# Performance work log

Measured on AMD Instinct MI355X. Metric: run time of the kernel, lower is better.

## Reference

```python
import jax, jax.numpy as jnp
import numpy as np


def setup_inputs() -> dict:
    key = jax.random.key(0)
    ks = jax.random.split(key, 7)
    B, S, D, F, E = 4, 2048, 1024, 4096, 8
    scale = 0.02
    return {
        "x": jax.random.normal(ks[0], (B, S, D), dtype=jnp.float32),
        "gate_w": jax.random.normal(ks[1], (D, E), dtype=jnp.float32) * scale,
        "gate_b": jnp.zeros((E,), dtype=jnp.float32),
        "w1": jax.random.normal(ks[2], (E, D, F), dtype=jnp.float32) * scale,
        "b1": jnp.zeros((E, F), dtype=jnp.float32),
        "w2": jax.random.normal(ks[3], (E, F, D), dtype=jnp.float32) * scale,
        "b2": jnp.zeros((E, D), dtype=jnp.float32),
        "top_k": 2,
    }


def reference(x, gate_w, gate_b, w1, b1, w2, b2, top_k):
    B, S, D = x.shape
    E = w1.shape[0]
    xf = x.reshape(-1, D)                      # [T, D], T = B*S
    T = xf.shape[0]

    # Router: top-k logits, softmax over the selected k (as in torch code)
    logits = xf @ gate_w + gate_b              # [T, E]
    rw, sel = jax.lax.top_k(logits, top_k)     # [T, k], [T, k]
    w = jax.nn.softmax(rw, axis=-1)            # [T, k]

    # Dense combine weights: combine[t, e] = sum_k w[t,k] * (sel[t,k]==e)
    combine = jnp.zeros((T, E), dtype=xf.dtype)
    combine = combine.at[jnp.arange(T)[:, None], sel].add(w)

    # Loop over small fixed expert count; each expert FFN on all tokens,
    # weighted by combine (zero for unrouted tokens). Dropout p honored as 0 (eval).
    out = jnp.zeros_like(xf)
    for e in range(E):
        h = jax.nn.gelu(xf @ w1[e] + b1[e], approximate=False)  # torch F.gelu = exact
        out = out + combine[:, e:e + 1] * (h @ w2[e] + b2[e])
    return out.reshape(B, S, D)
```

## Files before the change

kernel.cpp:

```cpp
#include <hip/hip_runtime.h>
#include <math.h>

#define T_TOK 8192
#define DDIM  1024
#define FDIM  4096
#define NEXP  8
#define MT256 72
#define NSLOT (2 * T_TOK)

typedef __attribute__((ext_vector_type(8))) short short8;
typedef __attribute__((ext_vector_type(4))) float f32x4;
typedef unsigned short u16;
typedef unsigned int   u32;

typedef const __attribute__((address_space(1))) u32* gp_t;
typedef       __attribute__((address_space(3))) u32* lp_t;

__device__ __forceinline__ void gload16(const void* g, void* l) {
  __builtin_amdgcn_global_load_lds((gp_t)g, (lp_t)l, 16, 0, 0);
}

#define VM0 asm volatile("s_waitcnt vmcnt(0)" ::: "memory")
#define SBAR __builtin_amdgcn_s_barrier()
#define SCHED0 __builtin_amdgcn_sched_barrier(0)

__device__ __forceinline__ u16 f2bf(float f) {
  u32 u = __float_as_uint(f);
  u = u + 0x7FFFu + ((u >> 16) & 1u);
  return (u16)(u >> 16);
}

__device__ __forceinline__ int imin(int a, int b) { return a < b ? a : b; }

__device__ __forceinline__ float gelu_fast(float v) {
  float u = 0.7978845608f * (v + 0.044715f * v * v * v);
  float t2 = __expf(2.f * u);
  float th = 1.f - 2.f / (t2 + 1.f);
  return 0.5f * v * (1.f + th);
}

__device__ __forceinline__ int xcd_swz(int orig, int nwg) {
  int xcd = orig & 7;
  int q = nwg >> 3, r = nwg & 7;
  int base = (xcd < r) ? xcd * (q + 1) : r * (q + 1) + (xcd - r) * q;
  return base + (orig >> 3);
}

__global__ __launch_bounds__(256) void router_kernel(
    const float* __restrict__ x, const float* __restrict__ gw,
    const float* __restrict__ gb, u16* __restrict__ xb,
    int* __restrict__ counts, int* __restrict__ sel, float* __restrict__ wts)
{
  const int t    = blockIdx.x * 4 + (threadIdx.x >> 6);
  const int lane = threadIdx.x & 63;
  const float* xr = x + (size_t)t * DDIM;
  u16* xbr = xb + (size_t)t * DDIM;
  float lg[NEXP];
  #pragma unroll
  for (int e = 0; e < NEXP; e++) lg[e] = 0.f;
  #pragma unroll
  for (int i = 0; i < 4; i++) {
    int d0 = i * 256 + lane * 4;
    float4 v = *(const float4*)(xr + d0);
    ushort4 o;
    o.x = f2bf(v.x); o.y = f2bf(v.y); o.z = f2bf(v.z); o.w = f2bf(v.w);
    *(ushort4*)(xbr + d0) = o;
    const float* g = gw + (size_t)d0 * NEXP;
    #pragma unroll
    for (int e = 0; e < NEXP; e++)
      lg[e] += v.x * g[e] + v.y * g[NEXP + e] + v.z * g[2 * NEXP + e] + v.w * g[3 * NEXP + e];
  }
  #pragma unroll
  for (int off = 32; off > 0; off >>= 1) {
    #pragma unroll
    for (int e = 0; e < NEXP; e++) lg[e] += __shfl_down(lg[e], off);
  }
  if (lane == 0) {
    float v0 = -1e30f, v1 = -1e30f; int s0 = 0, s1 = 0;
    #pragma unroll
    for (int e = 0; e < NEXP; e++) {
      float v = lg[e] + gb[e];
      if (v > v0) { v1 = v0; s1 = s0; v0 = v; s0 = e; }
      else if (v > v1) { v1 = v; s1 = e; }
    }
    float a  = expf(v1 - v0);
    float w0 = 1.f / (1.f + a);
    sel[t * 2] = s0; sel[t * 2 + 1] = s1;
    wts[t * 2] = w0; wts[t * 2 + 1] = 1.f - w0;
    atomicAdd(&counts[s0], 1); atomicAdd(&counts[s1], 1);
  }
}

__global__ __launch_bounds__(256) void scan_assign_kernel(
    const int* __restrict__ counts, const int* __restrict__ sel,
    const float* __restrict__ wts,
    int* __restrict__ offsets, int* __restrict__ map_e, int* __restrict__ map_r,
    int* __restrict__ nT, int* __restrict__ stok, float* __restrict__ swgt)
{
  __shared__ int spos[NEXP];
  if (threadIdx.x == 0) {
    int run = 0, nt = 0;
    for (int e = 0; e < NEXP; e++) {
      offsets[e] = run; spos[e] = run;
      int c = counts[e];
      int ntile = (c + 255) >> 8;
      for (int i = 0; i < ntile; i++) { map_e[nt] = e; map_r[nt] = i * 256; nt++; }
      run += c;
    }
    nT[0] = nt;
  }
  __syncthreads();
  for (int t = threadIdx.x; t < T_TOK; t += 256) {
    #pragma unroll
    for (int k = 0; k < 2; k++) {
      int e = sel[t * 2 + k];
      int p = atomicAdd(&spos[e], 1);
      stok[p] = t; swgt[p] = wts[t * 2 + k];
    }
  }
}

__global__ __launch_bounds__(256) void xgather_kernel(
    const u16* __restrict__ xb, const int* __restrict__ stok,
    u16* __restrict__ Xg)
{
  const int s = blockIdx.x * 2 + (threadIdx.x >> 7);
  const int u = threadIdx.x & 127;
  int tok = stok[s]; if ((u32)tok >= T_TOK) tok = 0;
  const uint4* src = (const uint4*)(xb + (size_t)tok * DDIM);
  uint4* dst = (uint4*)(Xg + (size_t)s * DDIM);
  dst[u] = src[u];
}

__global__ __launch_bounds__(256) void wtrans_kernel(
    const float* __restrict__ in, u16* __restrict__ out, int M, int N)
{
  const int e = blockIdx.z;
  in  += (size_t)e * M * N;
  out += (size_t)e * M * N;
  const int r0 = blockIdx.y * 128;
  const int c0 = blockIdx.x * 64;
  __shared__ float tile[128][65];
  const int tid = threadIdx.x;
  const int lr = tid >> 4;
  const int lc = (tid & 15) * 4;
  #pragma unroll
  for (int p = 0; p < 8; p++) {
    int r = p * 16 + lr;
    float4 v = *(const float4*)(in + (size_t)(r0 + r) * N + (c0 + lc));
    tile[r][lc] = v.x; tile[r][lc + 1] = v.y; tile[r][lc + 2] = v.z; tile[r][lc + 3] = v.w;
  }
  __syncthreads();
  const int oc = tid >> 4;
  const int om = (tid & 15) * 8;
  #pragma unroll
  for (int p = 0; p < 4; p++) {
    int c = p * 16 + oc;
    short8 o;
    #pragma unroll
    for (int j = 0; j < 8; j++) o[j] = (short)f2bf(tile[om + j][c]);
    *(short8*)(out + (size_t)(c0 + c) * M + (r0 + om)) = o;
  }
}

__global__ __launch_bounds__(512, 2) void gemm1_kernel(
    const u16* __restrict__ Xg, const u16* __restrict__ W1T,
    const float* __restrict__ B1,
    const int* __restrict__ counts, const int* __restrict__ offsets,
    const int* __restrict__ map_e, const int* __restrict__ map_r,
    const int* __restrict__ nT, u16* __restrict__ H)
{
  __shared__ __align__(16) char lds[2 * 65536];
  const int gid   = xcd_swz(blockIdx.x, gridDim.x);
  const int n_idx = gid / MT256;
  const int t_idx = gid - n_idx * MT256;
  if (t_idx >= nT[0]) return;
  const int e    = map_e[t_idx];
  const int row0 = map_r[t_idx];
  const int cnt  = counts[e];
  const int off  = offsets[e];
  const int n0   = n_idx * 256;

  const int tid = threadIdx.x, wave = tid >> 6, lane = tid & 63;
  const int lr = lane & 15, lq = lane >> 4;
  const int wr = wave >> 2, wc = wave & 3;
  const int l3 = lane >> 3;
  const int usrc = (lane & 7) ^ l3;

  const char* gA[4]; const char* gB[4];
  #pragma unroll
  for (int i = 0; i < 4; i++) {
    int rA = imin(off + row0 + wave * 32 + i * 8 + l3, NSLOT - 1);
    gA[i] = (const char*)Xg + (size_t)rA * 2048 + usrc * 16;
    int rB = e * FDIM + n0 + wave * 32 + i * 8 + l3;
    gB[i] = (const char*)W1T + (size_t)rB * 2048 + usrc * 16;
  }
  const int dbase = wave * 4096 + lane * 16;

  auto stage = [&](int buf, int kByte) {
    #pragma unroll
    for (int i = 0; i < 4; i++)
      gload16(gA[i] + kByte, lds + buf * 65536 + dbase + i * 1024);
    #pragma unroll
    for (int i = 0; i < 4; i++)
      gload16(gB[i] + kByte, lds + buf * 65536 + 32768 + dbase + i * 1024);
  };

  f32x4 acc[8][4] = {};
  auto compute = [&](int buf) {
    const u16* A  = (const u16*)(lds + buf * 65536);
    const u16* Bp = (const u16*)(lds + buf * 65536 + 32768);
    #pragma unroll
    for (int ks = 0; ks < 2; ks++) {
      const int uu = (((ks * 4 + lq) ^ (lr & 7))) * 8;
      short8 a[8], b[4];
      #pragma unroll
      for (int n = 0; n < 4; n++)
        b[n] = *(const short8*)&Bp[(wc * 64 + n * 16 + lr) * 64 + uu];
      #pragma unroll
      for (int m = 0; m < 8; m++)
        a[m] = *(const short8*)&A[(wr * 128 + m * 16 + lr) * 64 + uu];
      #pragma unroll
      for (int m = 0; m < 8; m++)
        #pragma unroll
        for (int n = 0; n < 4; n++)
          acc[m][n] = __builtin_amdgcn_mfma_f32_16x16x32_bf16(a[m], b[n], acc[m][n], 0, 0, 0);
    }
  };

  stage(0, 0);
  VM0; SCHED0; SBAR; SCHED0;
  #pragma unroll 1
  for (int t = 0; t < 16; t++) {
    if (t < 15) stage((t + 1) & 1, (t + 1) * 128);
    compute(t & 1);
    SCHED0; VM0; SCHED0; SBAR; SCHED0;
  }

  #pragma unroll
  for (int m = 0; m < 8; m++) {
    int rloc = wr * 128 + m * 16 + lq * 4;
    #pragma unroll
    for (int j = 0; j < 4; j++) {
      int r = rloc + j;
      if (row0 + r < cnt) {
        u16* Hrow = H + (size_t)(off + row0 + r) * FDIM;
        #pragma unroll
        for (int n = 0; n < 4; n++) {
          int col = n0 + wc * 64 + n * 16 + lr;
          float v = acc[m][n][j] + B1[e * FDIM + col];
          Hrow[col] = f2bf(gelu_fast(v));
        }
      }
    }
  }
}

__global__ __launch_bounds__(512, 2) void gemm2_kernel(
    const u16* __restrict__ H, const u16* __restrict__ W2T,
    const float* __restrict__ B2,
    const int* __restrict__ counts, const int* __restrict__ offsets,
    const int* __restrict__ slot_token, const float* __restrict__ slot_weight,
    const int* __restrict__ map_e, const int* __restrict__ map_r,
    const int* __restrict__ nT, float* __restrict__ out)
{
  __shared__ __align__(16) char lds[2 * 65536];
  const int gid   = xcd_swz(blockIdx.x, gridDim.x);
  const int sp    = gid / (4 * MT256);
  const int rem   = gid - sp * 4 * MT256;
  const int n_idx = rem / MT256;
  const int t_idx = rem - n_idx * MT256;
  if (t_idx >= nT[0]) return;
  const int e    = map_e[t_idx];
  const int row0 = map_r[t_idx];
  const int cnt  = counts[e];
  const int off  = offsets[e];
  const int n0   = n_idx * 256;
  const int kbase = sp * 4096;

  const int tid = threadIdx.x, wave = tid >> 6, lane = tid & 63;
  const int lr = lane & 15, lq = lane >> 4;
  const int wr = wave >> 2, wc = wave & 3;
  const int l3 = lane >> 3;
  const int usrc = (lane & 7) ^ l3;

  const char* gA[4]; const char* gB[4];
  #pragma unroll
  for (int i = 0; i < 4; i++) {
    int rA = imin(off + row0 + wave * 32 + i * 8 + l3, NSLOT - 1);
    gA[i] = (const char*)H + (size_t)rA * 8192 + kbase + usrc * 16;
    int rB = e * DDIM + n0 + wave * 32 + i * 8 + l3;
    gB[i] = (const char*)W2T + (size_t)rB * 8192 + kbase + usrc * 16;
  }
  const int dbase = wave * 4096 + lane * 16;

  auto stage = [&](int buf, int kByte) {
    #pragma unroll
    for (int i = 0; i < 4; i++)
      gload16(gA[i] + kByte, lds + buf * 65536 + dbase + i * 1024);
    #pragma unroll
    for (int i = 0; i < 4; i++)
      gload16(gB[i] + kByte, lds + buf * 65536 + 32768 + dbase + i * 1024);
  };

  f32x4 acc[8][4] = {};
  auto compute = [&](int buf) {
    const u16* A  = (const u16*)(lds + buf * 65536);
    const u16* Bp = (const u16*)(lds + buf * 65536 + 32768);
    #pragma unroll
    for (int ks = 0; ks < 2; ks++) {
      const int uu = (((ks * 4 + lq) ^ (lr & 7))) * 8;
      short8 a[8], b[4];
      #pragma unroll
      for (int n = 0; n < 4; n++)
        b[n] = *(const short8*)&Bp[(wc * 64 + n * 16 + lr) * 64 + uu];
      #pragma unroll
      for (int m = 0; m < 8; m++)
        a[m] = *(const short8*)&A[(wr * 128 + m * 16 + lr) * 64 + uu];
      #pragma unroll
      for (int m = 0; m < 8; m++)
        #pragma unroll
        for (int n = 0; n < 4; n++)
          acc[m][n] = __builtin_amdgcn_mfma_f32_16x16x32_bf16(a[m], b[n], acc[m][n], 0, 0, 0);
    }
  };

  stage(0, 0);
  VM0; SCHED0; SBAR; SCHED0;
  #pragma unroll 1
  for (int t = 0; t < 32; t++) {
    if (t < 31) stage((t + 1) & 1, (t + 1) * 128);
    compute(t & 1);
    SCHED0; VM0; SCHED0; SBAR; SCHED0;
  }

  #pragma unroll
  for (int m = 0; m < 8; m++) {
    int rloc = wr * 128 + m * 16 + lq * 4;
    #pragma unroll
    for (int j = 0; j < 4; j++) {
      int r = rloc + j;
      if (row0 + r >= cnt) continue;
      int s = off + row0 + r;
      int tok = slot_token[s];
      float wgt = slot_weight[s];
      #pragma unroll
      for (int n = 0; n < 4; n++) {
        int col = n0 + wc * 64 + n * 16 + lr;
        float v = acc[m][n][j];
        if (sp == 0) v += B2[e * DDIM + col];
        atomicAdd(&out[(size_t)tok * DDIM + col], wgt * v);
      }
    }
  }
}

extern "C" void kernel_launch(void* const* d_in, const int* in_sizes, int n_in,
                              void* d_out, int out_size, void* d_ws, size_t ws_size,
                              hipStream_t stream)
{
  (void)in_sizes; (void)n_in; (void)ws_size;
  const float* x  = (const float*)d_in[0];
  const float* gw = (const float*)d_in[1];
  const float* gb = (const float*)d_in[2];
  const float* w1 = (const float*)d_in[3];
  const float* b1 = (const float*)d_in[4];
  const float* w2 = (const float*)d_in[5];
  const float* b2 = (const float*)d_in[6];

  char* ws = (char*)d_ws;
  int*   counts = (int*)(ws + 0);
  int*   offp   = (int*)(ws + 64);
  int*   nT     = (int*)(ws + 128);
  int*   map_e  = (int*)(ws + 256);
  int*   map_r  = (int*)(ws + 1024);

  size_t p = 2048;
  int*   sel   = (int*)(ws + p);   p += (size_t)T_TOK * 2 * 4;
  float* wts   = (float*)(ws + p); p += (size_t)T_TOK * 2 * 4;
  int*   stok  = (int*)(ws + p);   p += (size_t)NSLOT * 4;
  float* swgt  = (float*)(ws + p); p += (size_t)NSLOT * 4;
  p = (p + 1048575) & ~(size_t)1048575;
  u16*   xb    = (u16*)(ws + p);   p += (size_t)T_TOK * DDIM * 2;
  u16*   Xg    = (u16*)(ws + p);   p += (size_t)NSLOT * DDIM * 2;
  u16*   w1t   = (u16*)(ws + p);   p += (size_t)NEXP * DDIM * FDIM * 2;
  u16*   w2t   = (u16*)(ws + p);   p += (size_t)NEXP * DDIM * FDIM * 2;
  u16*   Hbuf  = (u16*)(ws + p);

  hipMemsetAsync(ws, 0, 256, stream);
  hipMemsetAsync(d_out, 0, (size_t)out_size * sizeof(float), stream);
  router_kernel<<<T_TOK / 4, 256, 0, stream>>>(x, gw, gb, xb, counts, sel, wts);
  scan_assign_kernel<<<1, 256, 0, stream>>>(counts, sel, wts, offp, map_e, map_r, nT, stok, swgt);
  xgather_kernel<<<NSLOT / 2, 256, 0, stream>>>(xb, stok, Xg);
  wtrans_kernel<<<dim3(DDIM / 64, FDIM / 128, NEXP), 256, 0, stream>>>(w2, w2t, FDIM, DDIM);
  wtrans_kernel<<<dim3(FDIM / 64, DDIM / 128, NEXP), 256, 0, stream>>>(w1, w1t, DDIM, FDIM);

  gemm1_kernel<<<(FDIM / 256) * MT256, 512, 0, stream>>>(
      Xg, w1t, b1, counts, offp, map_e, map_r, nT, Hbuf);
  gemm2_kernel<<<2 * (DDIM / 256) * MT256, 512, 0, stream>>>(
      Hbuf, w2t, b2, counts, offp, stok, swgt, map_e, map_r, nT, (float*)d_out);
}
```

Baseline: 858.5 us.

## Use 128-row M tiles with triple-buffered LDS pipeline in expert GEMMs

Halves the token-tile height of both grouped GEMMs from 256 to 128 rows, so scan_assign emits 128-row tiles and the grids grow to a 136-tile maximum. This cuts padding waste on partially filled expert tiles and raises the block count. The LDS ring goes from two 64 KB buffers to three 48 KB slots, and loads are issued two stages ahead with a partial vmcnt wait instead of draining fully each step. In exchange, each B tile is loaded for half as many rows, so weight traffic per FLOP roughly doubles and per-wave MFMA work per iteration shrinks.

```diff
diff --git a/kernel.cpp b/kernel.cpp
--- a/kernel.cpp
+++ b/kernel.cpp
@@ -5,7 +5,7 @@
 #define DDIM  1024
 #define FDIM  4096
 #define NEXP  8
-#define MT256 72
+#define MAXT  136
 #define NSLOT (2 * T_TOK)
 
 typedef __attribute__((ext_vector_type(8))) short short8;
@@ -20,6 +20,7 @@
   __builtin_amdgcn_global_load_lds((gp_t)g, (lp_t)l, 16, 0, 0);
 }
 
+#define VM6 asm volatile("s_waitcnt vmcnt(6)" ::: "memory")
 #define VM0 asm volatile("s_waitcnt vmcnt(0)" ::: "memory")
 #define SBAR __builtin_amdgcn_s_barrier()
 #define SCHED0 __builtin_amdgcn_sched_barrier(0)
@@ -103,8 +104,8 @@
     for (int e = 0; e < NEXP; e++) {
       offsets[e] = run; spos[e] = run;
       int c = counts[e];
-      int ntile = (c + 255) >> 8;
-      for (int i = 0; i < ntile; i++) { map_e[nt] = e; map_r[nt] = i * 256; nt++; }
+      int ntile = (c + 127) >> 7;
+      for (int i = 0; i < ntile; i++) { map_e[nt] = e; map_r[nt] = i * 128; nt++; }
       run += c;
     }
     nT[0] = nt;
@@ -170,10 +171,10 @@
     const int* __restrict__ map_e, const int* __restrict__ map_r,
     const int* __restrict__ nT, u16* __restrict__ H)
 {
-  __shared__ __align__(16) char lds[2 * 65536];
+  __shared__ __align__(16) char lds[3 * 49152];
   const int gid   = xcd_swz(blockIdx.x, gridDim.x);
-  const int n_idx = gid / MT256;
-  const int t_idx = gid - n_idx * MT256;
+  const int n_idx = gid / MAXT;
+  const int t_idx = gid - n_idx * MAXT;
   if (t_idx >= nT[0]) return;
   const int e    = map_e[t_idx];
   const int row0 = map_r[t_idx];
@@ -187,59 +188,65 @@
   const int l3 = lane >> 3;
   const int usrc = (lane & 7) ^ l3;
 
-  const char* gA[4]; const char* gB[4];
+  const char* gA[2]; const char* gB[4];
+  #pragma unroll
+  for (int i = 0; i < 2; i++) {
+    int rA = imin(off + row0 + wave * 16 + i * 8 + l3, NSLOT - 1);
+    gA[i] = (const char*)Xg + (size_t)rA * 2048 + usrc * 16;
+  }
   #pragma unroll
   for (int i = 0; i < 4; i++) {
-    int rA = imin(off + row0 + wave * 32 + i * 8 + l3, NSLOT - 1);
-    gA[i] = (const char*)Xg + (size_t)rA * 2048 + usrc * 16;
     int rB = e * FDIM + n0 + wave * 32 + i * 8 + l3;
     gB[i] = (const char*)W1T + (size_t)rB * 2048 + usrc * 16;
   }
-  const int dbase = wave * 4096 + lane * 16;
-
-  auto stage = [&](int buf, int kByte) {
+
+  auto stage = [&](int slot, int kByte) {
+    char* base = lds + slot * 49152;
+    #pragma unroll
+    for (int i = 0; i < 2; i++)
+      gload16(gA[i] + kByte, base + wave * 2048 + i * 1024 + lane * 16);
     #pragma unroll
     for (int i = 0; i < 4; i++)
-      gload16(gA[i] + kByte, lds + buf * 65536 + dbase + i * 1024);
-    #pragma unroll
-    for (int i = 0; i < 4; i++)
-      gload16(gB[i] + kByte, lds + buf * 65536 + 32768 + dbase + i * 1024);
+      gload16(gB[i] + kByte, base + 16384 + wave * 4096 + i * 1024 + lane * 16);
   };
 
-  f32x4 acc[8][4] = {};
-  auto compute = [&](int buf) {
-    const u16* A  = (const u16*)(lds + buf * 65536);
-    const u16* Bp = (const u16*)(lds + buf * 65536 + 32768);
+  f32x4 acc[4][4] = {};
+  auto compute = [&](int slot) {
+    const u16* A  = (const u16*)(lds + slot * 49152);
+    const u16* Bp = (const u16*)(lds + slot * 49152 + 16384);
     #pragma unroll
     for (int ks = 0; ks < 2; ks++) {
-      const int uu = (((ks * 4 + lq) ^ (lr & 7))) * 8;
-      short8 a[8], b[4];
+      const int uu = ((ks * 4 + lq) ^ (lr & 7)) * 8;
+      short8 a[4], b[4];
       #pragma unroll
       for (int n = 0; n < 4; n++)
         b[n] = *(const short8*)&Bp[(wc * 64 + n * 16 + lr) * 64 + uu];
       #pragma unroll
-      for (int m = 0; m < 8; m++)
-        a[m] = *(const short8*)&A[(wr * 128 + m * 16 + lr) * 64 + uu];
-      #pragma unroll
-      for (int m = 0; m < 8; m++)
+      for (int m = 0; m < 4; m++)
+        a[m] = *(const short8*)&A[(wr * 64 + m * 16 + lr) * 64 + uu];
+      #pragma unroll
+      for (int m = 0; m < 4; m++)
         #pragma unroll
         for (int n = 0; n < 4; n++)
           acc[m][n] = __builtin_amdgcn_mfma_f32_16x16x32_bf16(a[m], b[n], acc[m][n], 0, 0, 0);
     }
   };
 
-  stage(0, 0);
-  VM0; SCHED0; SBAR; SCHED0;
+  stage(0, 0); stage(1, 128);
+  VM6; SCHED0; SBAR; SCHED0;
   #pragma unroll 1
   for (int t = 0; t < 16; t++) {
-    if (t < 15) stage((t + 1) & 1, (t + 1) * 128);
-    compute(t & 1);
-    SCHED0; VM0; SCHED0; SBAR; SCHED0;
-  }
-
-  #pragma unroll
-  for (int m = 0; m < 8; m++) {
-    int rloc = wr * 128 + m * 16 + lq * 4;
+    if (t + 2 < 16) stage((t + 2) % 3, (t + 2) * 128);
+    compute(t % 3);
+    SCHED0;
+    if (t + 2 < 16)       { VM6; }
+    else if (t + 2 == 16) { VM0; }
+    SCHED0; SBAR; SCHED0;
+  }
+
+  #pragma unroll
+  for (int m = 0; m < 4; m++) {
+    int rloc = wr * 64 + m * 16 + lq * 4;
     #pragma unroll
     for (int j = 0; j < 4; j++) {
       int r = rloc + j;
@@ -264,12 +271,12 @@
     const int* __restrict__ map_e, const int* __restrict__ map_r,
     const int* __restrict__ nT, float* __restrict__ out)
 {
-  __shared__ __align__(16) char lds[2 * 65536];
+  __shared__ __align__(16) char lds[3 * 49152];
   const int gid   = xcd_swz(blockIdx.x, gridDim.x);
-  const int sp    = gid / (4 * MT256);
-  const int rem   = gid - sp * 4 * MT256;
-  const int n_idx = rem / MT256;
-  const int t_idx = rem - n_idx * MT256;
+  const int sp    = gid / (4 * MAXT);
+  const int rem   = gid - sp * 4 * MAXT;
+  const int n_idx = rem / MAXT;
+  const int t_idx = rem - n_idx * MAXT;
   if (t_idx >= nT[0]) return;
   const int e    = map_e[t_idx];
   const int row0 = map_r[t_idx];
@@ -284,59 +291,65 @@
   const int l3 = lane >> 3;
   const int usrc = (lane & 7) ^ l3;
 
-  const char* gA[4]; const char* gB[4];
+  const char* gA[2]; const char* gB[4];
+  #pragma unroll
+  for (int i = 0; i < 2; i++) {
+    int rA = imin(off + row0 + wave * 16 + i * 8 + l3, NSLOT - 1);
+    gA[i] = (const char*)H + (size_t)rA * 8192 + kbase + usrc * 16;
+  }
   #pragma unroll
   for (int i = 0; i < 4; i++) {
-    int rA = imin(off + row0 + wave * 32 + i * 8 + l3, NSLOT - 1);
-    gA[i] = (const char*)H + (size_t)rA * 8192 + kbase + usrc * 16;
     int rB = e * DDIM + n0 + wave * 32 + i * 8 + l3;
     gB[i] = (const char*)W2T + (size_t)rB * 8192 + kbase + usrc * 16;
   }
-  const int dbase = wave * 4096 + lane * 16;
-
-  auto stage = [&](int buf, int kByte) {
+
+  auto stage = [&](int slot, int kByte) {
+    char* base = lds + slot * 49152;
+    #pragma unroll
+    for (int i = 0; i < 2; i++)
+      gload16(gA[i] + kByte, base + wave * 2048 + i * 1024 + lane * 16);
     #pragma unroll
     for (int i = 0; i < 4; i++)
-      gload16(gA[i] + kByte, lds + buf * 65536 + dbase + i * 1024);
-    #pragma unroll
-    for (int i = 0; i < 4; i++)
-      gload16(gB[i] + kByte, lds + buf * 65536 + 32768 + dbase + i * 1024);
+      gload16(gB[i] + kByte, base + 16384 + wave * 4096 + i * 1024 + lane * 16);
   };
 
-  f32x4 acc[8][4] = {};
-  auto compute = [&](int buf) {
-    const u16* A  = (const u16*)(lds + buf * 65536);
-    const u16* Bp = (const u16*)(lds + buf * 65536 + 32768);
+  f32x4 acc[4][4] = {};
+  auto compute = [&](int slot) {
+    const u16* A  = (const u16*)(lds + slot * 49152);
+    const u16* Bp = (const u16*)(lds + slot * 49152 + 16384);
     #pragma unroll
     for (int ks = 0; ks < 2; ks++) {
-      const int uu = (((ks * 4 + lq) ^ (lr & 7))) * 8;
-      short8 a[8], b[4];
+      const int uu = ((ks * 4 + lq) ^ (lr & 7)) * 8;
+      short8 a[4], b[4];
       #pragma unroll
       for (int n = 0; n < 4; n++)
         b[n] = *(const short8*)&Bp[(wc * 64 + n * 16 + lr) * 64 + uu];
       #pragma unroll
-      for (int m = 0; m < 8; m++)
-        a[m] = *(const short8*)&A[(wr * 128 + m * 16 + lr) * 64 + uu];
-      #pragma unroll
-      for (int m = 0; m < 8; m++)
+      for (int m = 0; m < 4; m++)
+        a[m] = *(const short8*)&A[(wr * 64 + m * 16 + lr) * 64 + uu];
+      #pragma unroll
+      for (int m = 0; m < 4; m++)
         #pragma unroll
         for (int n = 0; n < 4; n++)
           acc[m][n] = __builtin_amdgcn_mfma_f32_16x16x32_bf16(a[m], b[n], acc[m][n], 0, 0, 0);
     }
   };
 
-  stage(0, 0);
-  VM0; SCHED0; SBAR; SCHED0;
+  stage(0, 0); stage(1, 128);
+  VM6; SCHED0; SBAR; SCHED0;
   #pragma unroll 1
   for (int t = 0; t < 32; t++) {
-    if (t < 31) stage((t + 1) & 1, (t + 1) * 128);
-    compute(t & 1);
-    SCHED0; VM0; SCHED0; SBAR; SCHED0;
-  }
-
-  #pragma unroll
-  for (int m = 0; m < 8; m++) {
-    int rloc = wr * 128 + m * 16 + lq * 4;
+    if (t + 2 < 32) stage((t + 2) % 3, (t + 2) * 128);
+    compute(t % 3);
+    SCHED0;
+    if (t + 2 < 32)       { VM6; }
+    else if (t + 2 == 32) { VM0; }
+    SCHED0; SBAR; SCHED0;
+  }
+
+  #pragma unroll
+  for (int m = 0; m < 4; m++) {
+    int rloc = wr * 64 + m * 16 + lq * 4;
     #pragma unroll
     for (int j = 0; j < 4; j++) {
       int r = rloc + j;
@@ -395,8 +408,8 @@
   wtrans_kernel<<<dim3(DDIM / 64, FDIM / 128, NEXP), 256, 0, stream>>>(w2, w2t, FDIM, DDIM);
   wtrans_kernel<<<dim3(FDIM / 64, DDIM / 128, NEXP), 256, 0, stream>>>(w1, w1t, DDIM, FDIM);
 
-  gemm1_kernel<<<(FDIM / 256) * MT256, 512, 0, stream>>>(
+  gemm1_kernel<<<(FDIM / 256) * MAXT, 512, 0, stream>>>(
       Xg, w1t, b1, counts, offp, map_e, map_r, nT, Hbuf);
-  gemm2_kernel<<<2 * (DDIM / 256) * MT256, 512, 0, stream>>>(
+  gemm2_kernel<<<2 * (DDIM / 256) * MAXT, 512, 0, stream>>>(
       Hbuf, w2t, b2, counts, offp, stok, swgt, map_e, map_r, nT, (float*)d_out);
 }
```

Result: no change. 846.0 us (-1.5%).

## Split GEMM K-steps into four quadrant phases with fine-grained vmcnt waits

Applied to the files above, without the earlier changes.

Both expert GEMM kernels now issue the next tile's global-to-LDS loads in four quarter chunks, interleaved with four MFMA sub-blocks over 64x32 quadrants. Each chunk is followed by a partial s_waitcnt vmcnt(N) instead of a full drain at the end of each K step. LDS staging is rearranged so each chunk covers exactly the rows the next quadrant needs, and s_setprio is raised around MFMA bursts. The goal is to overlap memory latency with matrix math more finely, at the cost of more barriers per iteration and a riskier, hand-tuned wait-count schedule.

```diff
diff --git a/kernel.cpp b/kernel.cpp
--- a/kernel.cpp
+++ b/kernel.cpp
@@ -20,6 +20,10 @@
   __builtin_amdgcn_global_load_lds((gp_t)g, (lp_t)l, 16, 0, 0);
 }
 
+#define VM8 asm volatile("s_waitcnt vmcnt(8)" ::: "memory")
+#define VM6 asm volatile("s_waitcnt vmcnt(6)" ::: "memory")
+#define VM4 asm volatile("s_waitcnt vmcnt(4)" ::: "memory")
+#define VM2 asm volatile("s_waitcnt vmcnt(2)" ::: "memory")
 #define VM0 asm volatile("s_waitcnt vmcnt(0)" ::: "memory")
 #define SBAR __builtin_amdgcn_s_barrier()
 #define SCHED0 __builtin_amdgcn_sched_barrier(0)
@@ -163,6 +167,7 @@
   }
 }
 
+
 __global__ __launch_bounds__(512, 2) void gemm1_kernel(
     const u16* __restrict__ Xg, const u16* __restrict__ W1T,
     const float* __restrict__ B1,
@@ -184,58 +189,89 @@
   const int tid = threadIdx.x, wave = tid >> 6, lane = tid & 63;
   const int lr = lane & 15, lq = lane >> 4;
   const int wr = wave >> 2, wc = wave & 3;
-  const int l3 = lane >> 3;
-  const int usrc = (lane & 7) ^ l3;
-
-  const char* gA[4]; const char* gB[4];
-  #pragma unroll
-  for (int i = 0; i < 4; i++) {
-    int rA = imin(off + row0 + wave * 32 + i * 8 + l3, NSLOT - 1);
-    gA[i] = (const char*)Xg + (size_t)rA * 2048 + usrc * 16;
-    int rB = e * FDIM + n0 + wave * 32 + i * 8 + l3;
-    gB[i] = (const char*)W1T + (size_t)rB * 2048 + usrc * 16;
-  }
-  const int dbase = wave * 4096 + lane * 16;
-
-  auto stage = [&](int buf, int kByte) {
-    #pragma unroll
-    for (int i = 0; i < 4; i++)
-      gload16(gA[i] + kByte, lds + buf * 65536 + dbase + i * 1024);
-    #pragma unroll
-    for (int i = 0; i < 4; i++)
-      gload16(gB[i] + kByte, lds + buf * 65536 + 32768 + dbase + i * 1024);
-  };
+  const int l3 = lane >> 3, l7 = lane & 7;
+  const int usrc = l7 ^ l3;
+
+  const char* gAc[4]; const char* gBc[4];
+  int dA[4], dB[4];
+  #pragma unroll
+  for (int c = 0; c < 4; c++) {
+    int rbA = (c >> 1) * 64 + (c & 1) * 128 + wave * 8;
+    int sA  = imin(off + row0 + rbA + l3, NSLOT - 1);
+    gAc[c] = (const char*)Xg + (size_t)sA * 2048 + usrc * 16;
+    dA[c]  = rbA * 128 + lane * 16;
+    int rbB = (c >> 1) * 32 + ((c & 1) * 2 + (wave >> 2)) * 64 + (wave & 3) * 8;
+    gBc[c] = (const char*)W1T + (size_t)(e * FDIM + n0 + rbB + l3) * 2048 + usrc * 16;
+    dB[c]  = 32768 + rbB * 128 + lane * 16;
+  }
 
   f32x4 acc[8][4] = {};
-  auto compute = [&](int buf) {
-    const u16* A  = (const u16*)(lds + buf * 65536);
-    const u16* Bp = (const u16*)(lds + buf * 65536 + 32768);
-    #pragma unroll
-    for (int ks = 0; ks < 2; ks++) {
-      const int uu = (((ks * 4 + lq) ^ (lr & 7))) * 8;
-      short8 a[8], b[4];
-      #pragma unroll
-      for (int n = 0; n < 4; n++)
-        b[n] = *(const short8*)&Bp[(wc * 64 + n * 16 + lr) * 64 + uu];
-      #pragma unroll
-      for (int m = 0; m < 8; m++)
-        a[m] = *(const short8*)&A[(wr * 128 + m * 16 + lr) * 64 + uu];
-      #pragma unroll
-      for (int m = 0; m < 8; m++)
-        #pragma unroll
-        for (int n = 0; n < 4; n++)
-          acc[m][n] = __builtin_amdgcn_mfma_f32_16x16x32_bf16(a[m], b[n], acc[m][n], 0, 0, 0);
-    }
-  };
-
-  stage(0, 0);
-  VM0; SCHED0; SBAR; SCHED0;
+
+  #define STAGE_A1(buf, mh, kB) { \
+    gload16(gAc[(mh)*2]   + (kB), lds + (buf) * 65536 + dA[(mh)*2]);   \
+    gload16(gAc[(mh)*2+1] + (kB), lds + (buf) * 65536 + dA[(mh)*2+1]); }
+  #define STAGE_B1(buf, nh, kB) { \
+    gload16(gBc[(nh)*2]   + (kB), lds + (buf) * 65536 + dB[(nh)*2]);   \
+    gload16(gBc[(nh)*2+1] + (kB), lds + (buf) * 65536 + dB[(nh)*2+1]); }
+
+  #define LOAD_A1(buf, mh) { \
+    _Pragma("unroll") for (int ks = 0; ks < 2; ks++) { \
+      int uu = ((ks * 4 + lq) ^ (lr & 7)) * 16; \
+      _Pragma("unroll") for (int f = 0; f < 4; f++) \
+        a[f][ks] = *(const short8*)(lds + (buf) * 65536 + (wr * 128 + (mh) * 64 + f * 16 + lr) * 128 + uu); } }
+  #define LOAD_B1(buf, nh, bdst) { \
+    _Pragma("unroll") for (int ks = 0; ks < 2; ks++) { \
+      int uu = ((ks * 4 + lq) ^ (lr & 7)) * 16; \
+      _Pragma("unroll") for (int g = 0; g < 2; g++) \
+        bdst[g][ks] = *(const short8*)(lds + (buf) * 65536 + 32768 + (wc * 64 + (nh) * 32 + g * 16 + lr) * 128 + uu); } }
+
+  #define MFMA16(mh, nh, bsrc) { \
+    __builtin_amdgcn_s_setprio(1); \
+    _Pragma("unroll") for (int f = 0; f < 4; f++) \
+      _Pragma("unroll") for (int g = 0; g < 2; g++) \
+        _Pragma("unroll") for (int ks = 0; ks < 2; ks++) \
+          acc[(mh)*4+f][(nh)*2+g] = __builtin_amdgcn_mfma_f32_16x16x32_bf16(a[f][ks], bsrc[g][ks], acc[(mh)*4+f][(nh)*2+g], 0, 0, 0); \
+    __builtin_amdgcn_s_setprio(0); }
+
+  STAGE_A1(0, 0, 0); STAGE_B1(0, 0, 0); STAGE_B1(0, 1, 0); STAGE_A1(0, 1, 0);
+
+  const int NT = 16;
   #pragma unroll 1
-  for (int t = 0; t < 16; t++) {
-    if (t < 15) stage((t + 1) & 1, (t + 1) * 128);
-    compute(t & 1);
-    SCHED0; VM0; SCHED0; SBAR; SCHED0;
-  }
+  for (int t = 0; t < NT - 1; t++) {
+    const int buf = t & 1, nb = buf ^ 1;
+    const int kN = (t + 1) * 128;
+    short8 a[4][2], b0[2][2], b1[2][2];
+    STAGE_A1(nb, 0, kN); VM6; SCHED0; SBAR; SCHED0;
+    LOAD_A1(buf, 0); LOAD_B1(buf, 0, b0);
+    MFMA16(0, 0, b0); SCHED0; SBAR;
+    STAGE_B1(nb, 0, kN); VM6; SCHED0; SBAR; SCHED0;
+    LOAD_B1(buf, 1, b1);
+    MFMA16(0, 1, b1); SCHED0; SBAR;
+    STAGE_B1(nb, 1, kN); VM6; SCHED0; SBAR; SCHED0;
+    LOAD_A1(buf, 1);
+    MFMA16(1, 1, b1); SCHED0; SBAR;
+    STAGE_A1(nb, 1, kN); VM8; SCHED0; SBAR; SCHED0;
+    MFMA16(1, 0, b0); SCHED0; SBAR;
+  }
+  {
+    const int buf = (NT - 1) & 1;
+    short8 a[4][2], b0[2][2], b1[2][2];
+    VM4; SCHED0; SBAR; SCHED0;
+    LOAD_A1(buf, 0); LOAD_B1(buf, 0, b0);
+    MFMA16(0, 0, b0); SCHED0; SBAR;
+    VM2; SCHED0; SBAR; SCHED0;
+    LOAD_B1(buf, 1, b1);
+    MFMA16(0, 1, b1); SCHED0; SBAR;
+    VM0; SCHED0; SBAR; SCHED0;
+    LOAD_A1(buf, 1);
+    MFMA16(1, 1, b1); SCHED0; SBAR;
+    MFMA16(1, 0, b0);
+  }
+  #undef STAGE_A1
+  #undef STAGE_B1
+  #undef LOAD_A1
+  #undef LOAD_B1
+  #undef MFMA16
 
   #pragma unroll
   for (int m = 0; m < 8; m++) {
@@ -281,58 +317,87 @@
   const int tid = threadIdx.x, wave = tid >> 6, lane = tid & 63;
   const int lr = lane & 15, lq = lane >> 4;
   const int wr = wave >> 2, wc = wave & 3;
-  const int l3 = lane >> 3;
-  const int usrc = (lane & 7) ^ l3;
-
-  const char* gA[4]; const char* gB[4];
-  #pragma unroll
-  for (int i = 0; i < 4; i++) {
-    int rA = imin(off + row0 + wave * 32 + i * 8 + l3, NSLOT - 1);
-    gA[i] = (const char*)H + (size_t)rA * 8192 + kbase + usrc * 16;
-    int rB = e * DDIM + n0 + wave * 32 + i * 8 + l3;
-    gB[i] = (const char*)W2T + (size_t)rB * 8192 + kbase + usrc * 16;
-  }
-  const int dbase = wave * 4096 + lane * 16;
-
-  auto stage = [&](int buf, int kByte) {
-    #pragma unroll
-    for (int i = 0; i < 4; i++)
-      gload16(gA[i] + kByte, lds + buf * 65536 + dbase + i * 1024);
-    #pragma unroll
-    for (int i = 0; i < 4; i++)
-      gload16(gB[i] + kByte, lds + buf * 65536 + 32768 + dbase + i * 1024);
-  };
+  const int l3 = lane >> 3, l7 = lane & 7;
+  const int usrc = l7 ^ l3;
+
+  const char* gAc[4]; const char* gBc[4];
+  int dA[4], dB[4];
+  #pragma unroll
+  for (int c = 0; c < 4; c++) {
+    int rbA = (c >> 1) * 64 + (c & 1) * 128 + wave * 8;
+    int sA  = imin(off + row0 + rbA + l3, NSLOT - 1);
+    gAc[c] = (const char*)H + (size_t)sA * 8192 + kbase + usrc * 16;
+    dA[c]  = rbA * 128 + lane * 16;
+    int rbB = (c >> 1) * 32 + ((c & 1) * 2 + (wave >> 2)) * 64 + (wave & 3) * 8;
+    gBc[c] = (const char*)W2T + (size_t)(e * DDIM + n0 + rbB + l3) * 8192 + kbase + usrc * 16;
+    dB[c]  = 32768 + rbB * 128 + lane * 16;
+  }
 
   f32x4 acc[8][4] = {};
-  auto compute = [&](int buf) {
-    const u16* A  = (const u16*)(lds + buf * 65536);
-    const u16* Bp = (const u16*)(lds + buf * 65536 + 32768);
-    #pragma unroll
-    for (int ks = 0; ks < 2; ks++) {
-      const int uu = (((ks * 4 + lq) ^ (lr & 7))) * 8;
-      short8 a[8], b[4];
-      #pragma unroll
-      for (int n = 0; n < 4; n++)
-        b[n] = *(const short8*)&Bp[(wc * 64 + n * 16 + lr) * 64 + uu];
-      #pragma unroll
-      for (int m = 0; m < 8; m++)
-        a[m] = *(const short8*)&A[(wr * 128 + m * 16 + lr) * 64 + uu];
-      #pragma unroll
-      for (int m = 0; m < 8; m++)
-        #pragma unroll
-        for (int n = 0; n < 4; n++)
-          acc[m][n] = __builtin_amdgcn_mfma_f32_16x16x32_bf16(a[m], b[n], acc[m][n], 0, 0, 0);
-    }
-  };
-
-  stage(0, 0);
-  VM0; SCHED0; SBAR; SCHED0;
+
+  #define STAGE_A2(buf, mh, kB) { \
+    gload16(gAc[(mh)*2]   + (kB), lds + (buf) * 65536 + dA[(mh)*2]);   \
+    gload16(gAc[(mh)*2+1] + (kB), lds + (buf) * 65536 + dA[(mh)*2+1]); }
+  #define STAGE_B2(buf, nh, kB) { \
+    gload16(gBc[(nh)*2]   + (kB), lds + (buf) * 65536 + dB[(nh)*2]);   \
+    gload16(gBc[(nh)*2+1] + (kB), lds + (buf) * 65536 + dB[(nh)*2+1]); }
+  #define LOAD_A2(buf, mh) { \
+    _Pragma("unroll") for (int ks = 0; ks < 2; ks++) { \
+      int uu = ((ks * 4 + lq) ^ (lr & 7)) * 16; \
+      _Pragma("unroll") for (int f = 0; f < 4; f++) \
+        a[f][ks] = *(const short8*)(lds + (buf) * 65536 + (wr * 128 + (mh) * 64 + f * 16 + lr) * 128 + uu); } }
+  #define LOAD_B2(buf, nh, bdst) { \
+    _Pragma("unroll") for (int ks = 0; ks < 2; ks++) { \
+      int uu = ((ks * 4 + lq) ^ (lr & 7)) * 16; \
+      _Pragma("unroll") for (int g = 0; g < 2; g++) \
+        bdst[g][ks] = *(const short8*)(lds + (buf) * 65536 + 32768 + (wc * 64 + (nh) * 32 + g * 16 + lr) * 128 + uu); } }
+  #define MFMA16B(mh, nh, bsrc) { \
+    __builtin_amdgcn_s_setprio(1); \
+    _Pragma("unroll") for (int f = 0; f < 4; f++) \
+      _Pragma("unroll") for (int g = 0; g < 2; g++) \
+        _Pragma("unroll") for (int ks = 0; ks < 2; ks++) \
+          acc[(mh)*4+f][(nh)*2+g] = __builtin_amdgcn_mfma_f32_16x16x32_bf16(a[f][ks], bsrc[g][ks], acc[(mh)*4+f][(nh)*2+g], 0, 0, 0); \
+    __builtin_amdgcn_s_setprio(0); }
+
+  STAGE_A2(0, 0, 0); STAGE_B2(0, 0, 0); STAGE_B2(0, 1, 0); STAGE_A2(0, 1, 0);
+
+  const int NT = 32;
   #pragma unroll 1
-  for (int t = 0; t < 32; t++) {
-    if (t < 31) stage((t + 1) & 1, (t + 1) * 128);
-    compute(t & 1);
-    SCHED0; VM0; SCHED0; SBAR; SCHED0;
-  }
+  for (int t = 0; t < NT - 1; t++) {
+    const int buf = t & 1, nb = buf ^ 1;
+    const int kN = (t + 1) * 128;
+    short8 a[4][2], b0[2][2], b1[2][2];
+    STAGE_A2(nb, 0, kN); VM6; SCHED0; SBAR; SCHED0;
+    LOAD_A2(buf, 0); LOAD_B2(buf, 0, b0);
+    MFMA16B(0, 0, b0); SCHED0; SBAR;
+    STAGE_B2(nb, 0, kN); VM6; SCHED0; SBAR; SCHED0;
+    LOAD_B2(buf, 1, b1);
+    MFMA16B(0, 1, b1); SCHED0; SBAR;
+    STAGE_B2(nb, 1, kN); VM6; SCHED0; SBAR; SCHED0;
+    LOAD_A2(buf, 1);
+    MFMA16B(1, 1, b1); SCHED0; SBAR;
+    STAGE_A2(nb, 1, kN); VM8; SCHED0; SBAR; SCHED0;
+    MFMA16B(1, 0, b0); SCHED0; SBAR;
+  }
+  {
+    const int buf = (NT - 1) & 1;
+    short8 a[4][2], b0[2][2], b1[2][2];
+    VM4; SCHED0; SBAR; SCHED0;
+    LOAD_A2(buf, 0); LOAD_B2(buf, 0, b0);
+    MFMA16B(0, 0, b0); SCHED0; SBAR;
+    VM2; SCHED0; SBAR; SCHED0;
+    LOAD_B2(buf, 1, b1);
+    MFMA16B(0, 1, b1); SCHED0; SBAR;
+    VM0; SCHED0; SBAR; SCHED0;
+    LOAD_A2(buf, 1);
+    MFMA16B(1, 1, b1); SCHED0; SBAR;
+    MFMA16B(1, 0, b0);
+  }
+  #undef STAGE_A2
+  #undef STAGE_B2
+  #undef LOAD_A2
+  #undef LOAD_B2
+  #undef MFMA16B
 
   #pragma unroll
   for (int m = 0; m < 8; m++) {
```

Result: no change. 842.2 us (-1.9%).
